# Kernel tuning notes

Hardware: AMD Instinct MI355X
Metric: run time of the kernel (lower is better)

## Reference

```python
import jax, jax.numpy as jnp
import numpy as np

B, S, D, O, E, R, TOP_K = 4, 1024, 1024, 1024, 8, 16, 2
SCALING = 32.0 / 16.0  # lora_alpha / r
NEG_INF = -1e9  # stand-in for float('-inf'); exp underflows to 0 identically after softmax shift


def setup_inputs() -> dict:
    key = jax.random.key(0)
    ks = jax.random.split(key, 6)
    return {
        "x": jax.random.normal(ks[0], (B, S, D), jnp.float32),
        "base_w": jax.random.normal(ks[1], (O, D), jnp.float32) * 0.02,
        "base_b": jnp.zeros((O,), jnp.float32),
        "lora_A": jax.random.normal(ks[2], (E, D, R), jnp.float32) * 0.02,
        "lora_B": jax.random.normal(ks[3], (E, R, O), jnp.float32) * 0.02,
        "router_w": jax.random.normal(ks[4], (E, D), jnp.float32) * 0.02,
        "router_b": jnp.zeros((E,), jnp.float32),
    }


def reference(x, base_w, base_b, lora_A, lora_B, router_w, router_b):
    # base layer: F.linear(x, W, b)
    result = jnp.einsum('bsd,od->bso', x, base_w) + base_b
    # per-expert LoRA: ax = x @ A_e, bax = ax @ B_e
    ax = jnp.einsum('bsd,edr->bser', x, lora_A)        # [B,S,E,R]
    bax = jnp.einsum('bser,ero->bseo', ax, lora_B)     # [B,S,E,O]
    # linear router logits
    logits = jnp.einsum('bsd,ed->bse', x, router_w) + router_b  # [B,S,E]
    # top-k routing: mask logits below the k-th largest to -inf
    kth = jax.lax.top_k(logits, TOP_K)[0][..., -1:]
    masked = jnp.where(logits < kth, NEG_INF, logits)
    expert_weights = jax.nn.softmax(masked, axis=-1)   # [B,S,E]
    # combine experts, scale, add to base output
    return result + SCALING * jnp.einsum('bse,bseo->bso', expert_weights, bax)
```

## Files before the change

### kernel.cpp

```cpp
#include <hip/hip_runtime.h>
#include <cmath>

#define M_TOK 4096
#define KD    1024
#define KEXT  1152
#define NOUT  1024
#define ERDIM 128
#define SCALING 2.0f

typedef short bf16x8 __attribute__((ext_vector_type(8)));
typedef float f32x4  __attribute__((ext_vector_type(4)));

__device__ __forceinline__ ushort f2bf(float f) {
    union { float f; unsigned u; } v; v.f = f;
    unsigned r = v.u + 0x7fffu + ((v.u >> 16) & 1u);
    return (ushort)(r >> 16);
}
__device__ __forceinline__ float b2f(ushort u) {
    union { unsigned u; float f; } v; v.u = ((unsigned)u) << 16;
    return v.f;
}

typedef const unsigned int __attribute__((address_space(1)))* gas_ptr;
typedef unsigned int __attribute__((address_space(3)))* las_ptr;
__device__ __forceinline__ void gld_lds16(const ushort* g, ushort* l) {
    __builtin_amdgcn_global_load_lds((gas_ptr)g, (las_ptr)l, 16, 0, 0);
}


__global__ __launch_bounds__(256) void prep_router(
    const float* __restrict__ x, const float* __restrict__ rw,
    const float* __restrict__ rb, const float* __restrict__ base_w,
    const float* __restrict__ lora_A, const float* __restrict__ lora_B,
    ushort* __restrict__ Aext, ushort* __restrict__ Bpack,
    ushort* __restrict__ LATpack, float* __restrict__ wgt)
{
    const int tid = threadIdx.x;
    if (blockIdx.x >= 4096) {
        int i = (blockIdx.x - 4096) * 256 + tid;
        const int NB = NOUT * KEXT;
        if (i < NB) {
            int o = i / KEXT;
            int c = i - o * KEXT;
            float v = (c < KD) ? base_w[(size_t)o * KD + c]
                               : lora_B[(size_t)(c - KD) * NOUT + o];
            int lane = (o & 15) + ((c >> 3) & 3) * 16;
            int didx = (((o >> 4) * 36 + (c >> 5)) * 64 + lane) * 8 + (c & 7);
            Bpack[didx] = f2bf(v);
        } else {
            int j = i - NB;
            int er = j >> 10, d = j & 1023;
            int e = er >> 4, r = er & 15;
            float v = lora_A[((size_t)e * KD + d) * 16 + r];
            int lane = (er & 15) + ((d >> 3) & 3) * 16;
            int didx = (((er >> 4) * 32 + (d >> 5)) * 64 + lane) * 8 + (d & 7);
            LATpack[didx] = f2bf(v);
        }
        return;
    }
    const int t = blockIdx.x;
    const float4 xv = ((const float4*)(x + (size_t)t * KD))[tid];

    ushort4 xb;
    xb.x = f2bf(xv.x); xb.y = f2bf(xv.y); xb.z = f2bf(xv.z); xb.w = f2bf(xv.w);
    ((ushort4*)(Aext + (size_t)t * KEXT))[tid] = xb;

    double p[8];
    #pragma unroll
    for (int e = 0; e < 8; e++) {
        const float4 wv = ((const float4*)(rw + (size_t)e * KD))[tid];
        p[e] = (double)(xv.x * wv.x) + (double)(xv.y * wv.y) +
               (double)(xv.z * wv.z) + (double)(xv.w * wv.w);
    }

    const int wave = tid >> 6, lane = tid & 63;
    double q0, q1, q2, q3, r0, r1, s;
    {   const bool b = lane & 1;
        double s0 = b ? p[0] : p[1];
        double s1 = b ? p[2] : p[3];
        double s2 = b ? p[4] : p[5];
        double s3 = b ? p[6] : p[7];
        q0 = (b ? p[1] : p[0]) + __shfl_xor(s0, 1);
        q1 = (b ? p[3] : p[2]) + __shfl_xor(s1, 1);
        q2 = (b ? p[5] : p[4]) + __shfl_xor(s2, 1);
        q3 = (b ? p[7] : p[6]) + __shfl_xor(s3, 1);
    }
    {   const bool b = (lane >> 1) & 1;
        double s0 = b ? q0 : q1;
        double s1 = b ? q2 : q3;
        r0 = (b ? q1 : q0) + __shfl_xor(s0, 2);
        r1 = (b ? q3 : q2) + __shfl_xor(s1, 2);
    }
    {   const bool b = (lane >> 2) & 1;
        double s0 = b ? r0 : r1;
        s = (b ? r1 : r0) + __shfl_xor(s0, 4);
    }
    s += __shfl_xor(s, 8);
    s += __shfl_xor(s, 16);
    s += __shfl_xor(s, 32);

    __shared__ double red[4][8];
    __shared__ float  lg[8];
    if (lane < 8) red[wave][lane] = s;
    __syncthreads();
    if (tid < 8) {
        double sum = red[0][tid] + red[1][tid] + red[2][tid] + red[3][tid]
                   + (double)rb[tid];
        lg[tid] = (float)sum;
    }
    __syncthreads();
    if (tid < 8) {
        float my = lg[tid];
        float m1 = -INFINITY, m2 = -INFINITY;
        #pragma unroll
        for (int i = 0; i < 8; i++) {
            float v = lg[i];
            if (v > m1) { m2 = m1; m1 = v; }
            else if (v > m2) { m2 = v; }
        }
        float denom = 0.f;
        #pragma unroll
        for (int i = 0; i < 8; i++)
            if (lg[i] >= m2) denom += expf(lg[i] - m1);
        float w = (my >= m2) ? expf(my - m1) / denom : 0.f;
        wgt[t * 8 + tid] = SCALING * w;
    }
}

__global__ __launch_bounds__(256) void gemm_main(
    const ushort* __restrict__ A, const ushort* __restrict__ Bp,
    float* __restrict__ C, const float* __restrict__ bias)
{
    __shared__ __attribute__((aligned(16))) ushort As[2][128 * 64];

    const int tid  = threadIdx.x;
    const int wave = tid >> 6;
    const int lane = tid & 63;
    const int m0  = blockIdx.x * 128;
    const int ntb = blockIdx.y * 4;

    const int srow = tid >> 3;
    const int scol = ((tid & 7) ^ (srow & 7)) * 8;
    const ushort* aP = A + (size_t)(m0 + srow) * KEXT + scol;

    const int wr = wave * 32;
    const int fm = lane & 15;
    const int q  = lane >> 4;
    const int rx = fm & 7;

    const ushort* bBase = Bp + (size_t)lane * 8;

    f32x4 acc[2][4] = {};

    auto stageA = [&](int buf, int kk) {
        ushort* d = &As[buf][tid * 8];
        #pragma unroll
        for (int p = 0; p < 4; p++)
            gld_lds16(aP + kk + (size_t)(p * 32) * KEXT, d + p * 2048);
    };

    stageA(0, 0);

    for (int ks = 0; ks < 18; ++ks) {
        __syncthreads();
        if (ks + 1 < 18)
            stageA((ks + 1) & 1, (ks + 1) * 64);

        bf16x8 bf[2][4];
        #pragma unroll
        for (int kh = 0; kh < 2; kh++)
            #pragma unroll
            for (int ni = 0; ni < 4; ni++)
                bf[kh][ni] = *(const bf16x8*)(bBase +
                    (size_t)((ntb + ni) * 36 + ks * 2 + kh) * 512);

        const ushort* as = &As[ks & 1][0];
        bf16x8 af[2][2];
        #pragma unroll
        for (int kh = 0; kh < 2; kh++) {
            const int sg = ((kh * 4 + q) ^ rx) * 8;
            #pragma unroll
            for (int i = 0; i < 2; i++)
                af[kh][i] = *(const bf16x8*)&as[(wr + i * 16 + fm) * 64 + sg];
        }
        #pragma unroll
        for (int kh = 0; kh < 2; kh++)
            #pragma unroll
            for (int mi = 0; mi < 2; mi++)
                #pragma unroll
                for (int ni = 0; ni < 4; ni++)
                    acc[mi][ni] = __builtin_amdgcn_mfma_f32_16x16x32_bf16(
                        af[kh][mi], bf[kh][ni], acc[mi][ni], 0, 0, 0);
    }

    const int rr = q * 4;
    #pragma unroll
    for (int ni = 0; ni < 4; ni++) {
        const int col = (ntb + ni) * 16 + fm;
        const float bv = bias[col];
        #pragma unroll
        for (int mi = 0; mi < 2; mi++) {
            const int row = m0 + wr + mi * 16 + rr;
            #pragma unroll
            for (int r = 0; r < 4; r++)
                C[(size_t)(row + r) * NOUT + col] = acc[mi][ni][r] + bv;
        }
    }
}

__global__ __launch_bounds__(256) void gemm_ax(
    const ushort* __restrict__ A, const ushort* __restrict__ Lp,
    ushort* __restrict__ part)
{
    __shared__ __attribute__((aligned(16))) ushort As[2][64 * 64];

    const int tid  = threadIdx.x;
    const int wave = tid >> 6;
    const int lane = tid & 63;
    const int m0  = blockIdx.x * 64;
    const int kc0 = blockIdx.z * 8;
    part += (size_t)blockIdx.z * (M_TOK * ERDIM);

    const int srow = tid >> 3;
    const int scol = ((tid & 7) ^ (srow & 7)) * 8;
    const ushort* aP = A + (size_t)(m0 + srow) * KEXT + kc0 * 32 + scol;

    const int wr = (wave >> 1) * 32;
    const int wc = (wave & 1) * 64;
    const int fm = lane & 15;
    const int q  = lane >> 4;
    const int rx = fm & 7;

    const ushort* lBase = Lp + (size_t)lane * 8;
    const int ntw = (wave & 1) * 4;

    f32x4 acc[2][4] = {};

    auto stageA = [&](int buf, int kk) {
        ushort* d = &As[buf][tid * 8];
        #pragma unroll
        for (int p = 0; p < 2; p++)
            gld_lds16(aP + kk + (size_t)(p * 32) * KEXT, d + p * 2048);
    };

    stageA(0, 0);

    for (int ks = 0; ks < 4; ++ks) {
        __syncthreads();
        if (ks + 1 < 4)
            stageA((ks + 1) & 1, (ks + 1) * 64);

        bf16x8 bf[2][4];
        #pragma unroll
        for (int kh = 0; kh < 2; kh++)
            #pragma unroll
            for (int ni = 0; ni < 4; ni++)
                bf[kh][ni] = *(const bf16x8*)(lBase +
                    (size_t)((ntw + ni) * 32 + kc0 + ks * 2 + kh) * 512);

        const ushort* as = &As[ks & 1][0];
        bf16x8 af[2][2];
        #pragma unroll
        for (int kh = 0; kh < 2; kh++) {
            const int sg = ((kh * 4 + q) ^ rx) * 8;
            #pragma unroll
            for (int i = 0; i < 2; i++)
                af[kh][i] = *(const bf16x8*)&as[(wr + i * 16 + fm) * 64 + sg];
        }
        #pragma unroll
        for (int kh = 0; kh < 2; kh++)
            #pragma unroll
            for (int mi = 0; mi < 2; mi++)
                #pragma unroll
                for (int ni = 0; ni < 4; ni++)
                    acc[mi][ni] = __builtin_amdgcn_mfma_f32_16x16x32_bf16(
                        af[kh][mi], bf[kh][ni], acc[mi][ni], 0, 0, 0);
    }

    const int rr = q * 4;
    #pragma unroll
    for (int ni = 0; ni < 4; ni++) {
        const int col = wc + ni * 16 + fm;
        #pragma unroll
        for (int mi = 0; mi < 2; mi++) {
            const int row = m0 + wr + mi * 16 + rr;
            #pragma unroll
            for (int r = 0; r < 4; r++)
                part[(size_t)(row + r) * ERDIM + col] = f2bf(acc[mi][ni][r]);
        }
    }
}

__global__ __launch_bounds__(256) void ax_combine(
    const ushort* __restrict__ part, const float* __restrict__ wgt,
    ushort* __restrict__ Aext)
{
    int g = blockIdx.x * 256 + threadIdx.x;
    const int t = g >> 4, gr = g & 15;
    const int er0 = gr * 8;
    const int SL = M_TOK * ERDIM;
    const int base = t * ERDIM + er0;

    ushort4 p0a = *(const ushort4*)(part + base);
    ushort4 p0b = *(const ushort4*)(part + base + 4);
    ushort4 p1a = *(const ushort4*)(part + base + SL);
    ushort4 p1b = *(const ushort4*)(part + base + SL + 4);
    ushort4 p2a = *(const ushort4*)(part + base + 2 * SL);
    ushort4 p2b = *(const ushort4*)(part + base + 2 * SL + 4);
    ushort4 p3a = *(const ushort4*)(part + base + 3 * SL);
    ushort4 p3b = *(const ushort4*)(part + base + 3 * SL + 4);

    const float w = wgt[t * 8 + (er0 >> 4)];
    ushort o[8];
    o[0] = f2bf((b2f(p0a.x) + b2f(p1a.x) + b2f(p2a.x) + b2f(p3a.x)) * w);
    o[1] = f2bf((b2f(p0a.y) + b2f(p1a.y) + b2f(p2a.y) + b2f(p3a.y)) * w);
    o[2] = f2bf((b2f(p0a.z) + b2f(p1a.z) + b2f(p2a.z) + b2f(p3a.z)) * w);
    o[3] = f2bf((b2f(p0a.w) + b2f(p1a.w) + b2f(p2a.w) + b2f(p3a.w)) * w);
    o[4] = f2bf((b2f(p0b.x) + b2f(p1b.x) + b2f(p2b.x) + b2f(p3b.x)) * w);
    o[5] = f2bf((b2f(p0b.y) + b2f(p1b.y) + b2f(p2b.y) + b2f(p3b.y)) * w);
    o[6] = f2bf((b2f(p0b.z) + b2f(p1b.z) + b2f(p2b.z) + b2f(p3b.z)) * w);
    o[7] = f2bf((b2f(p0b.w) + b2f(p1b.w) + b2f(p2b.w) + b2f(p3b.w)) * w);

    ushort* dst = Aext + (size_t)t * KEXT + KD + er0;
    ((ushort4*)dst)[0] = *(ushort4*)&o[0];
    ((ushort4*)dst)[1] = *(ushort4*)&o[4];
}

extern "C" void kernel_launch(void* const* d_in, const int* in_sizes, int n_in,
                              void* d_out, int out_size, void* d_ws, size_t ws_size,
                              hipStream_t stream) {
    const float* x        = (const float*)d_in[0];
    const float* base_w   = (const float*)d_in[1];
    const float* base_b   = (const float*)d_in[2];
    const float* lora_A   = (const float*)d_in[3];
    const float* lora_B   = (const float*)d_in[4];
    const float* router_w = (const float*)d_in[5];
    const float* router_b = (const float*)d_in[6];
    float* out = (float*)d_out;

    char* ws = (char*)d_ws;
    ushort* Aext    = (ushort*)(ws);
    ushort* Bpack   = (ushort*)(ws + 9437184);
    ushort* LATpack = (ushort*)(ws + 11796480);
    float*  wgt     = (float*) (ws + 12058624);
    ushort* part    = (ushort*)(ws + 12189696);

    prep_router<<<9216, 256, 0, stream>>>(
        x, router_w, router_b, base_w, lora_A, lora_B,
        Aext, Bpack, LATpack, wgt);
    gemm_ax<<<dim3(64, 1, 4), 256, 0, stream>>>(Aext, LATpack, part);
    ax_combine<<<256, 256, 0, stream>>>(part, wgt, Aext);
    gemm_main<<<dim3(32, 16), 256, 0, stream>>>(Aext, Bpack, out, base_b);
}
```

Measured before the change: 125.2 us.

## Vectorize weight packing per output lane and prefetch B fragments across k-steps

The weight-packing blocks now assign each thread one 8-element packed fragment. Base weights are read with float4 loads and written as two ushort4 stores instead of scattered per-element writes, which cuts the packing grid from 5120 to 640 blocks. Both GEMMs now double-buffer the B fragments in registers, loading the next k-step's fragments before the current MFMAs to hide global load latency. This raises register pressure, and the per-element lora_B/lora_A reads are still strided.

```diff
diff --git a/kernel.cpp b/kernel.cpp
--- a/kernel.cpp
+++ b/kernel.cpp
@@ -37,24 +37,41 @@
 {
     const int tid = threadIdx.x;
     if (blockIdx.x >= 4096) {
-        int i = (blockIdx.x - 4096) * 256 + tid;
-        const int NB = NOUT * KEXT;
-        if (i < NB) {
-            int o = i / KEXT;
-            int c = i - o * KEXT;
-            float v = (c < KD) ? base_w[(size_t)o * KD + c]
-                               : lora_B[(size_t)(c - KD) * NOUT + o];
-            int lane = (o & 15) + ((c >> 3) & 3) * 16;
-            int didx = (((o >> 4) * 36 + (c >> 5)) * 64 + lane) * 8 + (c & 7);
-            Bpack[didx] = f2bf(v);
+        int tix = (blockIdx.x - 4096) * 256 + tid;
+        ushort v[8];
+        if (tix < 147456) {
+            const int lane = tix & 63;
+            const int tile = tix >> 6;
+            const int kc = tile % 36, ot = tile / 36;
+            const int o  = ot * 16 + (lane & 15);
+            const int c0 = kc * 32 + (lane >> 4) * 8;
+            if (c0 < KD) {
+                const float4* src = (const float4*)(base_w + (size_t)o * KD + c0);
+                float4 f0 = src[0], f1 = src[1];
+                v[0]=f2bf(f0.x); v[1]=f2bf(f0.y); v[2]=f2bf(f0.z); v[3]=f2bf(f0.w);
+                v[4]=f2bf(f1.x); v[5]=f2bf(f1.y); v[6]=f2bf(f1.z); v[7]=f2bf(f1.w);
+            } else {
+                #pragma unroll
+                for (int t = 0; t < 8; t++)
+                    v[t] = f2bf(lora_B[(size_t)(c0 + t - KD) * NOUT + o]);
+            }
+            ushort* dst = Bpack + (size_t)tix * 8;
+            ((ushort4*)dst)[0] = *(ushort4*)&v[0];
+            ((ushort4*)dst)[1] = *(ushort4*)&v[4];
         } else {
-            int j = i - NB;
-            int er = j >> 10, d = j & 1023;
-            int e = er >> 4, r = er & 15;
-            float v = lora_A[((size_t)e * KD + d) * 16 + r];
-            int lane = (er & 15) + ((d >> 3) & 3) * 16;
-            int didx = (((er >> 4) * 32 + (d >> 5)) * 64 + lane) * 8 + (d & 7);
-            LATpack[didx] = f2bf(v);
+            const int tix2 = tix - 147456;
+            const int lane = tix2 & 63;
+            const int tile = tix2 >> 6;
+            const int kc = tile & 31, nt = tile >> 5;
+            const int er = nt * 16 + (lane & 15);
+            const int d0 = kc * 32 + (lane >> 4) * 8;
+            const int e = er >> 4, r = er & 15;
+            #pragma unroll
+            for (int t = 0; t < 8; t++)
+                v[t] = f2bf(lora_A[((size_t)e * KD + d0 + t) * 16 + r]);
+            ushort* dst = LATpack + (size_t)tix2 * 8;
+            ((ushort4*)dst)[0] = *(ushort4*)&v[0];
+            ((ushort4*)dst)[1] = *(ushort4*)&v[4];
         }
         return;
     }
@@ -158,22 +175,25 @@
         for (int p = 0; p < 4; p++)
             gld_lds16(aP + kk + (size_t)(p * 32) * KEXT, d + p * 2048);
     };
-
-    stageA(0, 0);
-
-    for (int ks = 0; ks < 18; ++ks) {
-        __syncthreads();
-        if (ks + 1 < 18)
-            stageA((ks + 1) & 1, (ks + 1) * 64);
-
-        bf16x8 bf[2][4];
+    auto loadB = [&](bf16x8 (&bf)[2][4], int ks) {
         #pragma unroll
         for (int kh = 0; kh < 2; kh++)
             #pragma unroll
             for (int ni = 0; ni < 4; ni++)
                 bf[kh][ni] = *(const bf16x8*)(bBase +
                     (size_t)((ntb + ni) * 36 + ks * 2 + kh) * 512);
-
+    };
+
+    bf16x8 bfc[2][4], bfn[2][4];
+    stageA(0, 0);
+    loadB(bfc, 0);
+
+    for (int ks = 0; ks < 18; ++ks) {
+        __syncthreads();
+        if (ks + 1 < 18) {
+            loadB(bfn, ks + 1);
+            stageA((ks + 1) & 1, (ks + 1) * 64);
+        }
         const ushort* as = &As[ks & 1][0];
         bf16x8 af[2][2];
         #pragma unroll
@@ -190,7 +210,12 @@
                 #pragma unroll
                 for (int ni = 0; ni < 4; ni++)
                     acc[mi][ni] = __builtin_amdgcn_mfma_f32_16x16x32_bf16(
-                        af[kh][mi], bf[kh][ni], acc[mi][ni], 0, 0, 0);
+                        af[kh][mi], bfc[kh][ni], acc[mi][ni], 0, 0, 0);
+        #pragma unroll
+        for (int kh = 0; kh < 2; kh++)
+            #pragma unroll
+            for (int ni = 0; ni < 4; ni++)
+                bfc[kh][ni] = bfn[kh][ni];
     }
 
     const int rr = q * 4;
@@ -242,22 +267,25 @@
         for (int p = 0; p < 2; p++)
             gld_lds16(aP + kk + (size_t)(p * 32) * KEXT, d + p * 2048);
     };
-
-    stageA(0, 0);
-
-    for (int ks = 0; ks < 4; ++ks) {
-        __syncthreads();
-        if (ks + 1 < 4)
-            stageA((ks + 1) & 1, (ks + 1) * 64);
-
-        bf16x8 bf[2][4];
+    auto loadB = [&](bf16x8 (&bf)[2][4], int ks) {
         #pragma unroll
         for (int kh = 0; kh < 2; kh++)
             #pragma unroll
             for (int ni = 0; ni < 4; ni++)
                 bf[kh][ni] = *(const bf16x8*)(lBase +
                     (size_t)((ntw + ni) * 32 + kc0 + ks * 2 + kh) * 512);
-
+    };
+
+    bf16x8 bfc[2][4], bfn[2][4];
+    stageA(0, 0);
+    loadB(bfc, 0);
+
+    for (int ks = 0; ks < 4; ++ks) {
+        __syncthreads();
+        if (ks + 1 < 4) {
+            loadB(bfn, ks + 1);
+            stageA((ks + 1) & 1, (ks + 1) * 64);
+        }
         const ushort* as = &As[ks & 1][0];
         bf16x8 af[2][2];
         #pragma unroll
@@ -274,7 +302,12 @@
                 #pragma unroll
                 for (int ni = 0; ni < 4; ni++)
                     acc[mi][ni] = __builtin_amdgcn_mfma_f32_16x16x32_bf16(
-                        af[kh][mi], bf[kh][ni], acc[mi][ni], 0, 0, 0);
+                        af[kh][mi], bfc[kh][ni], acc[mi][ni], 0, 0, 0);
+        #pragma unroll
+        for (int kh = 0; kh < 2; kh++)
+            #pragma unroll
+            for (int ni = 0; ni < 4; ni++)
+                bfc[kh][ni] = bfn[kh][ni];
     }
 
     const int rr = q * 4;
@@ -345,7 +378,7 @@
     float*  wgt     = (float*) (ws + 12058624);
     ushort* part    = (ushort*)(ws + 12189696);
 
-    prep_router<<<9216, 256, 0, stream>>>(
+    prep_router<<<4736, 256, 0, stream>>>(
         x, router_w, router_b, base_w, lora_A, lora_B,
         Aext, Bpack, LATpack, wgt);
     gemm_ax<<<dim3(64, 1, 4), 256, 0, stream>>>(Aext, LATpack, part);
```

New measurement: 112.2 us. -10.4%, faster.
